# Performance work log

Measured on AMD Instinct MI355X. Metric: run time of the kernel, lower is better.

The kernel has to match this reference:

```python
import jax, jax.numpy as jnp
import numpy as np

N_NODES = 100000
N_EDGES = 1600000
NDIM_IN = 128
EDIMS = 64
NDIM_OUT = 128
NUM_HEADS = 4
HEAD_DIM = NDIM_OUT // NUM_HEADS


def setup_inputs() -> dict:
    key = jax.random.key(0)
    ks = jax.random.split(key, 10)
    in_dim = NDIM_IN + EDIMS
    # xavier-uniform style bounds for linear layers
    b1 = float(np.sqrt(6.0 / (in_dim + NDIM_OUT)))
    b2 = float(np.sqrt(6.0 / (NDIM_OUT + NDIM_OUT)))
    bav = float(np.sqrt(6.0 / (NUM_HEADS + HEAD_DIM)))
    return {
        "nfeats": jax.random.normal(ks[0], (N_NODES, NDIM_IN), dtype=jnp.float32),
        "efeats": jax.random.normal(ks[1], (N_EDGES, EDIMS), dtype=jnp.float32),
        "src": jax.random.randint(ks[2], (N_EDGES,), 0, N_NODES, dtype=jnp.int32),
        "dst": jax.random.randint(ks[3], (N_EDGES,), 0, N_NODES, dtype=jnp.int32),
        "W_proj_w": jax.random.uniform(ks[4], (NDIM_OUT, in_dim), jnp.float32, -b1, b1),
        "W_proj_b": jnp.zeros((NDIM_OUT,), jnp.float32),
        "attn_vec": jax.random.uniform(ks[5], (NUM_HEADS, HEAD_DIM), jnp.float32, -bav, bav),
        "W_out_w": jax.random.uniform(ks[6], (NDIM_OUT, NDIM_OUT), jnp.float32, -b2, b2),
        "W_out_b": jnp.zeros((NDIM_OUT,), jnp.float32),
        "ln_gamma": jnp.ones((NDIM_OUT,), jnp.float32),
        "ln_beta": jnp.zeros((NDIM_OUT,), jnp.float32),
    }


def reference(nfeats, efeats, src, dst, W_proj_w, W_proj_b, attn_vec,
              W_out_w, W_out_b, ln_gamma, ln_beta):
    N = nfeats.shape[0]
    H, D = attn_vec.shape  # num_heads, head_dim
    # gather src node feats + edge feats, project: [E, H, D]
    x = jnp.concatenate([nfeats[src], efeats], axis=1)
    x_proj = (x @ W_proj_w.T + W_proj_b).reshape(-1, H, D)
    # per-head attention scores: [E, H]
    e = jnp.sum(x_proj * attn_vec, axis=-1)
    # edge softmax grouped by destination node (numerically stable)
    emax = jax.ops.segment_max(e, dst, num_segments=N)  # [N, H]
    ex = jnp.exp(e - emax[dst])
    denom = jax.ops.segment_sum(ex, dst, num_segments=N)  # [N, H]
    alpha = ex / denom[dst]  # [E, H]
    # weighted messages, scatter-sum to destination nodes
    # (dropout is identity at inference)
    m = (x_proj * alpha[:, :, None]).reshape(-1, H * D)  # [E, ndim_out]
    h_neigh = jax.ops.segment_sum(m, dst, num_segments=N)  # [N, ndim_out]
    # W_resid is Identity since ndim_in == ndim_out
    h = jax.nn.relu((h_neigh + nfeats) @ W_out_w.T + W_out_b)
    # layernorm
    mu = jnp.mean(h, axis=-1, keepdims=True)
    var = jnp.mean((h - mu) ** 2, axis=-1, keepdims=True)
    return (h - mu) * jax.lax.rsqrt(var + 1e-5) * ln_gamma + ln_beta
```

## Files before the change

kernel.cpp:

```cpp
#include <hip/hip_runtime.h>
#include <math.h>

#define NN 100000
#define NE 1600000
#define F 128
#define EF 64
#define NH 4
#define HD 32

__global__ void k_prep_c(const float* __restrict__ Wp, const float* __restrict__ av,
                         float* __restrict__ c) {
    int t = threadIdx.x;
    int h = t >> 6;
    int j = t & 63;
    float acc = 0.f;
#pragma unroll
    for (int d = 0; d < HD; ++d)
        acc += Wp[(h * HD + d) * 192 + 128 + j] * av[h * HD + d];
    c[h * EF + j] = acc;
}

__global__ __launch_bounds__(256, 3) void k_node_proj(
    const float* __restrict__ nf, const float* __restrict__ Wp,
    const float* __restrict__ bp, float* __restrict__ P) {
    __shared__ float in_t[32][129];
    __shared__ float w_t[64][129];
    int t = threadIdx.x;
    int nb = blockIdx.x * 32;
#pragma unroll
    for (int i = 0; i < 4; ++i) {
        int f4 = i * 256 + t;
        int row = f4 >> 5, c4 = f4 & 31;
        float4 v = ((const float4*)(nf + (size_t)(nb + row) * F))[c4];
        in_t[row][c4 * 4 + 0] = v.x; in_t[row][c4 * 4 + 1] = v.y;
        in_t[row][c4 * 4 + 2] = v.z; in_t[row][c4 * 4 + 3] = v.w;
    }
    int kk = t & 63, ng = t >> 6;
    for (int kh = 0; kh < 2; ++kh) {
        __syncthreads();
#pragma unroll
        for (int i = 0; i < 8; ++i) {
            int f4 = i * 256 + t;
            int row = f4 >> 5, c4 = f4 & 31;
            float4 v = *(const float4*)(Wp + (size_t)(kh * 64 + row) * 192 + c4 * 4);
            w_t[row][c4 * 4 + 0] = v.x; w_t[row][c4 * 4 + 1] = v.y;
            w_t[row][c4 * 4 + 2] = v.z; w_t[row][c4 * 4 + 3] = v.w;
        }
        __syncthreads();
        float acc[8] = {0.f, 0.f, 0.f, 0.f, 0.f, 0.f, 0.f, 0.f};
        for (int j = 0; j < 128; ++j) {
            float w = w_t[kk][j];
#pragma unroll
            for (int i = 0; i < 8; ++i)
                acc[i] += in_t[ng * 8 + i][j] * w;
        }
        float b = bp[kh * 64 + kk];
#pragma unroll
        for (int i = 0; i < 8; ++i)
            P[(size_t)(nb + ng * 8 + i) * F + kh * 64 + kk] = acc[i] + b;
    }
}

__global__ void k_sn(const float* __restrict__ P, const float* __restrict__ av,
                     float* __restrict__ sn) {
    __shared__ __align__(16) float avs[128];
    int t = threadIdx.x;
    if (t < 128) avs[t] = av[t];
    __syncthreads();
    int n = blockIdx.x * 64 + (t >> 2);
    int h = t & 3;
    if (n >= NN) return;
    const float* p = P + (size_t)n * F + h * HD;
    const float* a = avs + h * HD;
    float acc = 0.f;
#pragma unroll
    for (int q = 0; q < 8; ++q) {
        float4 v = ((const float4*)p)[q];
        float4 w = ((const float4*)a)[q];
        acc += v.x * w.x + v.y * w.y + v.z * w.z + v.w * w.w;
    }
    sn[n * 4 + h] = acc;
}

__global__ __launch_bounds__(256, 2) void k_edge_score(
    const float* __restrict__ ef, const int* __restrict__ src,
    const int* __restrict__ dst, const float* __restrict__ sn,
    const float* __restrict__ c, float* __restrict__ ex,
    float* __restrict__ denom) {
    __shared__ float eft[256][65];
    __shared__ float cs[4][64];
    int t = threadIdx.x;
    int eb = blockIdx.x * 256;
    cs[t >> 6][t & 63] = c[t];
#pragma unroll
    for (int i = 0; i < 16; ++i) {
        int f4 = i * 256 + t;
        int row = f4 >> 4, c4 = f4 & 15;
        float4 v = ((const float4*)(ef + (size_t)(eb + row) * EF))[c4];
        eft[row][c4 * 4 + 0] = v.x; eft[row][c4 * 4 + 1] = v.y;
        eft[row][c4 * 4 + 2] = v.z; eft[row][c4 * 4 + 3] = v.w;
    }
    __syncthreads();
    int e = eb + t;
    int s = src[e], d = dst[e];
    float4 snv = *(const float4*)(sn + (size_t)s * 4);
    float a0 = snv.x, a1 = snv.y, a2 = snv.z, a3 = snv.w;
    for (int j = 0; j < 64; ++j) {
        float x = eft[t][j];
        a0 += x * cs[0][j];
        a1 += x * cs[1][j];
        a2 += x * cs[2][j];
        a3 += x * cs[3][j];
    }
    float e0 = __expf(a0), e1 = __expf(a1), e2 = __expf(a2), e3 = __expf(a3);
    float4 exv = make_float4(e0, e1, e2, e3);
    *(float4*)(ex + (size_t)e * 4) = exv;
    atomicAdd(&denom[d * 4 + 0], e0);
    atomicAdd(&denom[d * 4 + 1], e1);
    atomicAdd(&denom[d * 4 + 2], e2);
    atomicAdd(&denom[d * 4 + 3], e3);
}

__global__ __launch_bounds__(256, 3) void k_edge_msg(
    const float* __restrict__ ef, const int* __restrict__ src,
    const int* __restrict__ dst, const float* __restrict__ Wp,
    const float* __restrict__ P, const float* __restrict__ ex,
    const float* __restrict__ denom, float* __restrict__ hne) {
    __shared__ float eft[64][65];
    __shared__ float wt[128][65];
    int t = threadIdx.x;
    int eb = blockIdx.x * 64;
#pragma unroll
    for (int i = 0; i < 8; ++i) {
        int f4 = i * 256 + t;
        int row = f4 >> 4, c4 = f4 & 15;
        float4 v = *(const float4*)(Wp + (size_t)row * 192 + 128 + c4 * 4);
        wt[row][c4 * 4 + 0] = v.x; wt[row][c4 * 4 + 1] = v.y;
        wt[row][c4 * 4 + 2] = v.z; wt[row][c4 * 4 + 3] = v.w;
    }
#pragma unroll
    for (int i = 0; i < 4; ++i) {
        int f4 = i * 256 + t;
        int row = f4 >> 4, c4 = f4 & 15;
        float4 v = ((const float4*)(ef + (size_t)(eb + row) * EF))[c4];
        eft[row][c4 * 4 + 0] = v.x; eft[row][c4 * 4 + 1] = v.y;
        eft[row][c4 * 4 + 2] = v.z; eft[row][c4 * 4 + 3] = v.w;
    }
    __syncthreads();
    int et = t >> 4;
    int kt = t & 15;
    int e0 = et * 4;
    float acc[4][8] = {};
    for (int j = 0; j < 64; ++j) {
        float efr[4];
#pragma unroll
        for (int i = 0; i < 4; ++i) efr[i] = eft[e0 + i][j];
#pragma unroll
        for (int m = 0; m < 8; ++m) {
            float w = wt[m * 16 + kt][j];
#pragma unroll
            for (int i = 0; i < 4; ++i)
                acc[i][m] += efr[i] * w;
        }
    }
#pragma unroll
    for (int i = 0; i < 4; ++i) {
        int e = eb + e0 + i;
        int s = src[e], d = dst[e];
        float4 exv = *(const float4*)(ex + (size_t)e * 4);
        float4 dnv = *(const float4*)(denom + (size_t)d * 4);
        float al[4] = {exv.x / dnv.x, exv.y / dnv.y, exv.z / dnv.z, exv.w / dnv.w};
        const float* pr = P + (size_t)s * F;
        float* hr = hne + (size_t)d * F;
#pragma unroll
        for (int m = 0; m < 8; ++m) {
            int k = m * 16 + kt;
            float mv = al[k >> 5] * (pr[k] + acc[i][m]);
            atomicAdd(&hr[k], mv);
        }
    }
}

__global__ __launch_bounds__(256, 2) void k_node_out(
    const float* __restrict__ hne, const float* __restrict__ nf,
    const float* __restrict__ Wo, const float* __restrict__ bo,
    const float* __restrict__ gamma, const float* __restrict__ beta,
    float* __restrict__ out) {
    __shared__ float in_t[32][129];
    __shared__ float w_t[64][129];
    __shared__ float h_t[32][132];
    int t = threadIdx.x;
    int nb = blockIdx.x * 32;
#pragma unroll
    for (int i = 0; i < 4; ++i) {
        int f4 = i * 256 + t;
        int row = f4 >> 5, c4 = f4 & 31;
        float4 a = ((const float4*)(hne + (size_t)(nb + row) * F))[c4];
        float4 b = ((const float4*)(nf + (size_t)(nb + row) * F))[c4];
        in_t[row][c4 * 4 + 0] = a.x + b.x; in_t[row][c4 * 4 + 1] = a.y + b.y;
        in_t[row][c4 * 4 + 2] = a.z + b.z; in_t[row][c4 * 4 + 3] = a.w + b.w;
    }
    int kk = t & 63, ng = t >> 6;
    for (int kh = 0; kh < 2; ++kh) {
        __syncthreads();
#pragma unroll
        for (int i = 0; i < 8; ++i) {
            int f4 = i * 256 + t;
            int row = f4 >> 5, c4 = f4 & 31;
            float4 v = ((const float4*)(Wo + (size_t)(kh * 64 + row) * F))[c4];
            w_t[row][c4 * 4 + 0] = v.x; w_t[row][c4 * 4 + 1] = v.y;
            w_t[row][c4 * 4 + 2] = v.z; w_t[row][c4 * 4 + 3] = v.w;
        }
        __syncthreads();
        float acc[8] = {0.f, 0.f, 0.f, 0.f, 0.f, 0.f, 0.f, 0.f};
        for (int j = 0; j < 128; ++j) {
            float w = w_t[kk][j];
#pragma unroll
            for (int i = 0; i < 8; ++i)
                acc[i] += in_t[ng * 8 + i][j] * w;
        }
        float b = bo[kh * 64 + kk];
#pragma unroll
        for (int i = 0; i < 8; ++i) {
            float v = acc[i] + b;
            h_t[ng * 8 + i][kh * 64 + kk] = v > 0.f ? v : 0.f;
        }
    }
    __syncthreads();
    int n = t >> 3, li = t & 7;
    float s = 0.f, ss = 0.f;
    float vals[16];
#pragma unroll
    for (int q = 0; q < 16; ++q) {
        float v = h_t[n][li * 16 + q];
        vals[q] = v; s += v; ss += v * v;
    }
#pragma unroll
    for (int o = 1; o < 8; o <<= 1) {
        s += __shfl_xor(s, o, 64);
        ss += __shfl_xor(ss, o, 64);
    }
    float mu = s * (1.f / 128.f);
    float var = ss * (1.f / 128.f) - mu * mu;
    float rstd = rsqrtf(var + 1e-5f);
    float* orow = out + (size_t)(nb + n) * F + li * 16;
#pragma unroll
    for (int q4 = 0; q4 < 4; ++q4) {
        float4 o;
        int k = li * 16 + q4 * 4;
        o.x = (vals[q4 * 4 + 0] - mu) * rstd * gamma[k + 0] + beta[k + 0];
        o.y = (vals[q4 * 4 + 1] - mu) * rstd * gamma[k + 1] + beta[k + 1];
        o.z = (vals[q4 * 4 + 2] - mu) * rstd * gamma[k + 2] + beta[k + 2];
        o.w = (vals[q4 * 4 + 3] - mu) * rstd * gamma[k + 3] + beta[k + 3];
        *(float4*)(orow + q4 * 4) = o;
    }
}

extern "C" void kernel_launch(void* const* d_in, const int* in_sizes, int n_in,
                              void* d_out, int out_size, void* d_ws, size_t ws_size,
                              hipStream_t stream) {
    const float* nf    = (const float*)d_in[0];
    const float* ef    = (const float*)d_in[1];
    const int*   src   = (const int*)d_in[2];
    const int*   dst   = (const int*)d_in[3];
    const float* Wp    = (const float*)d_in[4];
    const float* bp    = (const float*)d_in[5];
    const float* av    = (const float*)d_in[6];
    const float* Wo    = (const float*)d_in[7];
    const float* bo    = (const float*)d_in[8];
    const float* gamma = (const float*)d_in[9];
    const float* beta  = (const float*)d_in[10];
    float* out = (float*)d_out;

    float* P     = (float*)d_ws;
    float* sn    = P + (size_t)NN * F;
    float* c     = sn + (size_t)NN * 4;
    float* denom = c + 256;
    float* ex    = denom + (size_t)NN * 4;
    float* hne   = ex + (size_t)NE * 4;

    hipMemsetAsync(denom, 0, (size_t)NN * 4 * sizeof(float), stream);
    hipMemsetAsync(hne, 0, (size_t)NN * F * sizeof(float), stream);

    k_prep_c<<<1, 256, 0, stream>>>(Wp, av, c);
    k_node_proj<<<NN / 32, 256, 0, stream>>>(nf, Wp, bp, P);
    k_sn<<<(NN + 63) / 64, 256, 0, stream>>>(P, av, sn);
    k_edge_score<<<NE / 256, 256, 0, stream>>>(ef, src, dst, sn, c, ex, denom);
    k_edge_msg<<<NE / 64, 256, 0, stream>>>(ef, src, dst, Wp, P, ex, denom, hne);
    k_node_out<<<NN / 32, 256, 0, stream>>>(hne, nf, Wo, bo, gamma, beta, out);
}
```

Measured before the change: 1.907 ms.

## Sort edges by destination into CSR and aggregate per node without atomics

Builds a CSR ordering of edges by destination (histogram, three-stage scan, scatter) and replaces the separate edge-score and edge-message kernels with one per-node aggregation kernel. Each block owns 32 destination nodes, recomputes scores, exponentials and the edge-feature projection for its edges, and accumulates the softmax denominator and messages in registers. This removes the float atomics into denom and hne, the ex buffer round trip and the hne memset. In exchange it adds CSR-build kernels with integer atomics, gathers edge features in random order, and stages projected edge features in bf16 shared memory, which reduces precision. Softmax still skips the max subtraction, as before.

```diff
diff --git a/kernel.cpp b/kernel.cpp
--- a/kernel.cpp
+++ b/kernel.cpp
@@ -1,4 +1,5 @@
 #include <hip/hip_runtime.h>
+#include <hip/hip_bf16.h>
 #include <math.h>
 
 #define NN 100000
@@ -7,6 +8,7 @@
 #define EF 64
 #define NH 4
 #define HD 32
+#define SCAN_NBLK 98
 
 __global__ void k_prep_c(const float* __restrict__ Wp, const float* __restrict__ av,
                          float* __restrict__ c) {
@@ -82,54 +84,90 @@
     sn[n * 4 + h] = acc;
 }
 
-__global__ __launch_bounds__(256, 2) void k_edge_score(
+__global__ void k_hist(const int* __restrict__ dst, int* __restrict__ cnt) {
+    int e = blockIdx.x * 256 + threadIdx.x;
+    if (e < NE) atomicAdd(&cnt[dst[e]], 1);
+}
+
+__global__ void k_scan_a(const int* __restrict__ cnt, int* __restrict__ ro,
+                         int* __restrict__ bsum) {
+    __shared__ int buf[256];
+    int t = threadIdx.x;
+    int base = blockIdx.x * 1024 + t * 4;
+    int v0 = 0, v1 = 0, v2 = 0, v3 = 0;
+    if (base + 0 < NN) v0 = cnt[base + 0];
+    if (base + 1 < NN) v1 = cnt[base + 1];
+    if (base + 2 < NN) v2 = cnt[base + 2];
+    if (base + 3 < NN) v3 = cnt[base + 3];
+    int s = v0 + v1 + v2 + v3;
+    buf[t] = s;
+    __syncthreads();
+    for (int off = 1; off < 256; off <<= 1) {
+        int x = (t >= off) ? buf[t - off] : 0;
+        __syncthreads();
+        buf[t] += x;
+        __syncthreads();
+    }
+    int run = buf[t] - s;
+    if (base + 0 < NN) ro[base + 0] = run; run += v0;
+    if (base + 1 < NN) ro[base + 1] = run; run += v1;
+    if (base + 2 < NN) ro[base + 2] = run; run += v2;
+    if (base + 3 < NN) ro[base + 3] = run;
+    if (t == 255) bsum[blockIdx.x] = buf[255];
+}
+
+__global__ void k_scan_b(const int* __restrict__ bsum, int* __restrict__ boff) {
+    __shared__ int buf[128];
+    int t = threadIdx.x;
+    int v = (t < SCAN_NBLK) ? bsum[t] : 0;
+    buf[t] = v;
+    __syncthreads();
+    for (int off = 1; off < 128; off <<= 1) {
+        int x = (t >= off) ? buf[t - off] : 0;
+        __syncthreads();
+        buf[t] += x;
+        __syncthreads();
+    }
+    if (t < SCAN_NBLK) boff[t] = buf[t] - v;
+}
+
+__global__ void k_scan_c(int* __restrict__ ro, const int* __restrict__ boff) {
+    int base = blockIdx.x * 1024 + threadIdx.x * 4;
+    int add = boff[blockIdx.x];
+#pragma unroll
+    for (int i = 0; i < 4; ++i)
+        if (base + i < NN) ro[base + i] += add;
+    if (blockIdx.x == 0 && threadIdx.x == 0) ro[NN] = NE;
+}
+
+__global__ void k_scatter(const int* __restrict__ dst, const int* __restrict__ ro,
+                          int* __restrict__ rank, int* __restrict__ perm) {
+    int e = blockIdx.x * 256 + threadIdx.x;
+    if (e < NE) {
+        int d = dst[e];
+        int r = atomicAdd(&rank[d], 1);
+        perm[ro[d] + r] = e;
+    }
+}
+
+__global__ __launch_bounds__(256, 2) void k_agg2(
     const float* __restrict__ ef, const int* __restrict__ src,
-    const int* __restrict__ dst, const float* __restrict__ sn,
-    const float* __restrict__ c, float* __restrict__ ex,
-    float* __restrict__ denom) {
-    __shared__ float eft[256][65];
+    const int* __restrict__ perm, const int* __restrict__ row_off,
+    const float* __restrict__ Wp, const float* __restrict__ P,
+    const float* __restrict__ sn, const float* __restrict__ c,
+    float* __restrict__ hne) {
+    __shared__ float wt[128][65];
+    __shared__ float eft[64][65];
+    __shared__ __hip_bfloat16 qt[64][132];
+    __shared__ float ext[64][4];
     __shared__ float cs[4][64];
-    int t = threadIdx.x;
-    int eb = blockIdx.x * 256;
-    cs[t >> 6][t & 63] = c[t];
-#pragma unroll
-    for (int i = 0; i < 16; ++i) {
-        int f4 = i * 256 + t;
-        int row = f4 >> 4, c4 = f4 & 15;
-        float4 v = ((const float4*)(ef + (size_t)(eb + row) * EF))[c4];
-        eft[row][c4 * 4 + 0] = v.x; eft[row][c4 * 4 + 1] = v.y;
-        eft[row][c4 * 4 + 2] = v.z; eft[row][c4 * 4 + 3] = v.w;
-    }
-    __syncthreads();
-    int e = eb + t;
-    int s = src[e], d = dst[e];
-    float4 snv = *(const float4*)(sn + (size_t)s * 4);
-    float a0 = snv.x, a1 = snv.y, a2 = snv.z, a3 = snv.w;
-    for (int j = 0; j < 64; ++j) {
-        float x = eft[t][j];
-        a0 += x * cs[0][j];
-        a1 += x * cs[1][j];
-        a2 += x * cs[2][j];
-        a3 += x * cs[3][j];
-    }
-    float e0 = __expf(a0), e1 = __expf(a1), e2 = __expf(a2), e3 = __expf(a3);
-    float4 exv = make_float4(e0, e1, e2, e3);
-    *(float4*)(ex + (size_t)e * 4) = exv;
-    atomicAdd(&denom[d * 4 + 0], e0);
-    atomicAdd(&denom[d * 4 + 1], e1);
-    atomicAdd(&denom[d * 4 + 2], e2);
-    atomicAdd(&denom[d * 4 + 3], e3);
-}
-
-__global__ __launch_bounds__(256, 3) void k_edge_msg(
-    const float* __restrict__ ef, const int* __restrict__ src,
-    const int* __restrict__ dst, const float* __restrict__ Wp,
-    const float* __restrict__ P, const float* __restrict__ ex,
-    const float* __restrict__ denom, float* __restrict__ hne) {
-    __shared__ float eft[64][65];
-    __shared__ float wt[128][65];
-    int t = threadIdx.x;
-    int eb = blockIdx.x * 64;
+    __shared__ int ro[33];
+    __shared__ int eidx[64];
+    __shared__ int sarr[64];
+
+    int t = threadIdx.x;
+    int nb = blockIdx.x * 32;
+
 #pragma unroll
     for (int i = 0; i < 8; ++i) {
         int f4 = i * 256 + t;
@@ -138,46 +176,90 @@
         wt[row][c4 * 4 + 0] = v.x; wt[row][c4 * 4 + 1] = v.y;
         wt[row][c4 * 4 + 2] = v.z; wt[row][c4 * 4 + 3] = v.w;
     }
-#pragma unroll
-    for (int i = 0; i < 4; ++i) {
-        int f4 = i * 256 + t;
-        int row = f4 >> 4, c4 = f4 & 15;
-        float4 v = ((const float4*)(ef + (size_t)(eb + row) * EF))[c4];
-        eft[row][c4 * 4 + 0] = v.x; eft[row][c4 * 4 + 1] = v.y;
-        eft[row][c4 * 4 + 2] = v.z; eft[row][c4 * 4 + 3] = v.w;
-    }
-    __syncthreads();
-    int et = t >> 4;
-    int kt = t & 15;
-    int e0 = et * 4;
-    float acc[4][8] = {};
-    for (int j = 0; j < 64; ++j) {
-        float efr[4];
-#pragma unroll
-        for (int i = 0; i < 4; ++i) efr[i] = eft[e0 + i][j];
-#pragma unroll
-        for (int m = 0; m < 8; ++m) {
-            float w = wt[m * 16 + kt][j];
-#pragma unroll
-            for (int i = 0; i < 4; ++i)
-                acc[i][m] += efr[i] * w;
-        }
-    }
-#pragma unroll
-    for (int i = 0; i < 4; ++i) {
-        int e = eb + e0 + i;
-        int s = src[e], d = dst[e];
-        float4 exv = *(const float4*)(ex + (size_t)e * 4);
-        float4 dnv = *(const float4*)(denom + (size_t)d * 4);
-        float al[4] = {exv.x / dnv.x, exv.y / dnv.y, exv.z / dnv.z, exv.w / dnv.w};
-        const float* pr = P + (size_t)s * F;
-        float* hr = hne + (size_t)d * F;
-#pragma unroll
-        for (int m = 0; m < 8; ++m) {
-            int k = m * 16 + kt;
-            float mv = al[k >> 5] * (pr[k] + acc[i][m]);
-            atomicAdd(&hr[k], mv);
-        }
+    cs[t >> 6][t & 63] = c[t];
+    if (t < 33) ro[t] = row_off[nb + t];
+    __syncthreads();
+
+    int e_begin = ro[0], e_end = ro[32];
+    int kt = t & 15, et = t >> 4, e0 = et * 4;
+    int hh = t >> 6, es = t & 63;
+    int n_own = t >> 3, q0 = (t & 7) * 16;
+    int own_lo = ro[n_own], own_hi = ro[n_own + 1];
+    int hown = q0 >> 5;
+    float S[16] = {0.f, 0.f, 0.f, 0.f, 0.f, 0.f, 0.f, 0.f,
+                   0.f, 0.f, 0.f, 0.f, 0.f, 0.f, 0.f, 0.f};
+    float den = 0.f;
+
+    for (int ce = e_begin; ce < e_end; ce += 64) {
+        int m = min(64, e_end - ce);
+        if (t < m) {
+            int pe = perm[ce + t];
+            eidx[t] = pe;
+            sarr[t] = src[pe];
+        }
+        __syncthreads();
+#pragma unroll
+        for (int i = 0; i < 4; ++i) {
+            int f4 = i * 256 + t;
+            int row = f4 >> 4, c4 = f4 & 15;
+            if (row < m) {
+                float4 v = ((const float4*)(ef + (size_t)eidx[row] * EF))[c4];
+                eft[row][c4 * 4 + 0] = v.x; eft[row][c4 * 4 + 1] = v.y;
+                eft[row][c4 * 4 + 2] = v.z; eft[row][c4 * 4 + 3] = v.w;
+            }
+        }
+        __syncthreads();
+        if (es < m) {
+            float a = sn[(size_t)sarr[es] * 4 + hh];
+            const float* crow = cs[hh];
+#pragma unroll 8
+            for (int j = 0; j < 64; ++j) a += eft[es][j] * crow[j];
+            ext[es][hh] = __expf(a);
+        }
+        float acc[4][8] = {};
+        for (int j = 0; j < 64; ++j) {
+            float f0 = eft[e0 + 0][j], f1 = eft[e0 + 1][j];
+            float f2 = eft[e0 + 2][j], f3 = eft[e0 + 3][j];
+#pragma unroll
+            for (int mm = 0; mm < 8; ++mm) {
+                float w = wt[mm * 16 + kt][j];
+                acc[0][mm] += f0 * w; acc[1][mm] += f1 * w;
+                acc[2][mm] += f2 * w; acc[3][mm] += f3 * w;
+            }
+        }
+#pragma unroll
+        for (int i = 0; i < 4; ++i)
+#pragma unroll
+            for (int mm = 0; mm < 8; ++mm)
+                qt[e0 + i][mm * 16 + kt] = __float2bfloat16(acc[i][mm]);
+        __syncthreads();
+        {
+            int lo = max(own_lo, ce), hi = min(own_hi, ce + m);
+            for (int e = lo; e < hi; ++e) {
+                int el = e - ce;
+                float exv = ext[el][hown];
+                const float* pr = P + (size_t)sarr[el] * F + q0;
+                den += exv;
+#pragma unroll
+                for (int q = 0; q < 16; q += 4) {
+                    float4 pv = *(const float4*)(pr + q);
+                    S[q + 0] += exv * (pv.x + __bfloat162float(qt[el][q0 + q + 0]));
+                    S[q + 1] += exv * (pv.y + __bfloat162float(qt[el][q0 + q + 1]));
+                    S[q + 2] += exv * (pv.z + __bfloat162float(qt[el][q0 + q + 2]));
+                    S[q + 3] += exv * (pv.w + __bfloat162float(qt[el][q0 + q + 3]));
+                }
+            }
+        }
+        __syncthreads();
+    }
+    float rd = den > 0.f ? 1.f / den : 0.f;
+    float* orow = hne + (size_t)(nb + n_own) * F + q0;
+#pragma unroll
+    for (int q = 0; q < 16; q += 4) {
+        float4 o;
+        o.x = S[q + 0] * rd; o.y = S[q + 1] * rd;
+        o.z = S[q + 2] * rd; o.w = S[q + 3] * rd;
+        *(float4*)(orow + q) = o;
     }
 }
 
@@ -272,20 +354,30 @@
     const float* beta  = (const float*)d_in[10];
     float* out = (float*)d_out;
 
-    float* P     = (float*)d_ws;
-    float* sn    = P + (size_t)NN * F;
-    float* c     = sn + (size_t)NN * 4;
-    float* denom = c + 256;
-    float* ex    = denom + (size_t)NN * 4;
-    float* hne   = ex + (size_t)NE * 4;
-
-    hipMemsetAsync(denom, 0, (size_t)NN * 4 * sizeof(float), stream);
-    hipMemsetAsync(hne, 0, (size_t)NN * F * sizeof(float), stream);
+    float* P      = (float*)d_ws;
+    float* sn     = P + (size_t)NN * F;
+    float* c      = sn + (size_t)NN * 4;
+    float* hne    = c + 256;
+    int* cnt      = (int*)(hne + (size_t)NN * F);
+    int* rank     = cnt + NN;
+    int* row_off  = rank + NN;
+    int* bsum     = row_off + NN + 1;
+    int* boff     = bsum + 128;
+    int* perm     = boff + 128;
+
+    hipMemsetAsync(cnt, 0, (size_t)NN * sizeof(int), stream);
+    hipMemsetAsync(rank, 0, (size_t)NN * sizeof(int), stream);
 
     k_prep_c<<<1, 256, 0, stream>>>(Wp, av, c);
     k_node_proj<<<NN / 32, 256, 0, stream>>>(nf, Wp, bp, P);
     k_sn<<<(NN + 63) / 64, 256, 0, stream>>>(P, av, sn);
-    k_edge_score<<<NE / 256, 256, 0, stream>>>(ef, src, dst, sn, c, ex, denom);
-    k_edge_msg<<<NE / 64, 256, 0, stream>>>(ef, src, dst, Wp, P, ex, denom, hne);
+
+    k_hist<<<(NE + 255) / 256, 256, 0, stream>>>(dst, cnt);
+    k_scan_a<<<SCAN_NBLK, 256, 0, stream>>>(cnt, row_off, bsum);
+    k_scan_b<<<1, 128, 0, stream>>>(bsum, boff);
+    k_scan_c<<<SCAN_NBLK, 256, 0, stream>>>(row_off, boff);
+    k_scatter<<<(NE + 255) / 256, 256, 0, stream>>>(dst, row_off, rank, perm);
+
+    k_agg2<<<NN / 32, 256, 0, stream>>>(ef, src, perm, row_off, Wp, P, sn, c, hne);
     k_node_out<<<NN / 32, 256, 0, stream>>>(hne, nf, Wo, bo, gamma, beta, out);
 }
```

Result: slower. 1.960 ms (+2.7%).
